# Kernel tuning notes

Measured on AMD Instinct MI355X. Metric: run time of the kernel, lower is better.

## Reference

```python
import jax, jax.numpy as jnp
import numpy as np

N_NODES = 100000
N_EDGES = 1600000
EMB_DIM = 32
NUM_LAYERS = 3


def setup_inputs() -> dict:
    key = jax.random.key(0)
    k_emb, k_w, k_row, k_col = jax.random.split(key, 4)
    emb = jax.random.normal(k_emb, (N_NODES, EMB_DIM), dtype=jnp.float32)
    # positive normalized edge weights (stands in for 1/sqrt(d1*d2))
    edge_weight = jax.random.uniform(k_w, (N_EDGES,), dtype=jnp.float32)
    row = jax.random.randint(k_row, (N_EDGES,), 0, N_NODES, dtype=jnp.int32)
    col = jax.random.randint(k_col, (N_EDGES,), 0, N_NODES, dtype=jnp.int32)
    return {"emb": emb, "edge_weight": edge_weight, "row": row, "col": col,
            "num_layers": NUM_LAYERS}


def reference(emb, edge_weight, row, col, num_layers):
    # Repeated SpMM: out[row] += w * X[col], equivalent to
    # torch.sparse.mm(sparse_coo(stack([row,col]), w, (N,N)), X)
    n = emb.shape[0]
    w = edge_weight[:, None]  # [E, 1]
    X = emb
    for _ in range(num_layers):
        msgs = w * X[col]  # gather + scale, [E, d]
        X = jax.ops.segment_sum(msgs, row, num_segments=n)
    return X
```

## Files before the change

kernel.cpp:

```cpp
#include <hip/hip_runtime.h>

#define EMB_DIM 32
#define CB_SHIFT 10
#define CB_ROWS 1024
#define COLBITS 17
#define OCT 8
#define EPB 4096
#define P1_T 256
#define SCAN_T 256
#define SCAN_E 8
#define SCAN_BLOCK (SCAN_T * SCAN_E)

__device__ __forceinline__ unsigned short f2b(float f) {
    unsigned u = __float_as_uint(f);
    u += 0x7fffu + ((u >> 16) & 1u);
    return (unsigned short)(u >> 16);
}
__device__ __forceinline__ unsigned f2b2(float lo, float hi) {
    return (unsigned)f2b(lo) | ((unsigned)f2b(hi) << 16);
}
__device__ __forceinline__ float blo(unsigned u) { return __uint_as_float(u << 16); }
__device__ __forceinline__ float bhi(unsigned u) { return __uint_as_float(u & 0xffff0000u); }


__global__ void coarse_count(const int* __restrict__ row, int* __restrict__ C,
                             int n_edges, int ncb, int nblk) {
    __shared__ int h[128];
    const int t = threadIdx.x;
    if (t < 128) h[t] = 0;
    __syncthreads();
    const int base = blockIdx.x * EPB;
    const int end = min(base + EPB, n_edges);
    for (int i = base + t; i < end; i += P1_T)
        atomicAdd(&h[row[i] >> CB_SHIFT], 1);
    __syncthreads();
    if (t < ncb) C[t * nblk + blockIdx.x] = h[t];
}


__global__ void scan_block_sums(const int* __restrict__ C, int* __restrict__ bsum, int M) {
    const int base = blockIdx.x * SCAN_BLOCK;
    const int t = threadIdx.x;
    int s = 0;
#pragma unroll
    for (int i = 0; i < SCAN_E; ++i) {
        int idx = base + i * SCAN_T + t;
        if (idx < M) s += C[idx];
    }
    __shared__ int red[SCAN_T];
    red[t] = s;
    __syncthreads();
    for (int d = SCAN_T / 2; d > 0; d >>= 1) {
        if (t < d) red[t] += red[t + d];
        __syncthreads();
    }
    if (t == 0) bsum[blockIdx.x] = red[0];
}

__global__ void scan_bsum(int* __restrict__ bsum, int nbs, int* __restrict__ off, int n_nodes) {
    __shared__ int sh[SCAN_T];
    const int t = threadIdx.x;
    int carry = 0;
    for (int base = 0; base < nbs; base += SCAN_T) {
        int v = (base + t < nbs) ? bsum[base + t] : 0;
        sh[t] = v;
        __syncthreads();
        for (int d = 1; d < SCAN_T; d <<= 1) {
            int add = (t >= d) ? sh[t - d] : 0;
            __syncthreads();
            sh[t] += add;
            __syncthreads();
        }
        if (base + t < nbs) bsum[base + t] = carry + sh[t] - v;
        int chunk_total = sh[SCAN_T - 1];
        __syncthreads();
        carry += chunk_total;
    }
    if (t == 0) off[n_nodes] = carry;
}

__global__ void scan_block_write(int* __restrict__ C, const int* __restrict__ bbase, int M) {
    const int base = blockIdx.x * SCAN_BLOCK;
    const int t = threadIdx.x;
    const int lo = base + t * SCAN_E;
    int vals[SCAN_E];
#pragma unroll
    for (int i = 0; i < SCAN_E; ++i) {
        int idx = lo + i;
        vals[i] = (idx < M) ? C[idx] : 0;
    }
    int tsum = 0;
#pragma unroll
    for (int i = 0; i < SCAN_E; ++i) tsum += vals[i];

    __shared__ int sh[SCAN_T];
    sh[t] = tsum;
    __syncthreads();
    for (int d = 1; d < SCAN_T; d <<= 1) {
        int add = (t >= d) ? sh[t - d] : 0;
        __syncthreads();
        sh[t] += add;
        __syncthreads();
    }
    int run = bbase[blockIdx.x] + sh[t] - tsum;
#pragma unroll
    for (int i = 0; i < SCAN_E; ++i) {
        int idx = lo + i;
        if (idx < M) C[idx] = run;
        run += vals[i];
    }
}

__global__ void coarse_scatter(const int* __restrict__ row, const int* __restrict__ col,
                               const float* __restrict__ w, const int* __restrict__ O,
                               int2* __restrict__ ebuf, int n_edges, int ncb, int nblk) {
    __shared__ int cur[128];
    const int t = threadIdx.x;
    if (t < ncb) cur[t] = O[t * nblk + blockIdx.x];
    __syncthreads();
    const int base = blockIdx.x * EPB;
    const int end = min(base + EPB, n_edges);
    for (int i = base + t; i < end; i += P1_T) {
        int r = row[i];
        int pos = atomicAdd(&cur[r >> CB_SHIFT], 1);
        ebuf[pos] = make_int2(((r & (CB_ROWS - 1)) << COLBITS) | col[i], __float_as_int(w[i]));
    }
}

__global__ void fine_localize(const int2* __restrict__ ebuf, const int* __restrict__ O,
                              int ncb, int nblk, int n_edges,
                              int2* __restrict__ colw, int* __restrict__ off, int n_nodes) {
    const int b = blockIdx.x;
    const int base = O[b * nblk];
    const int endp = (b + 1 < ncb) ? O[(b + 1) * nblk] : n_edges;
    const int t = threadIdx.x;

    __shared__ int cnt[CB_ROWS * OCT];
    __shared__ int cur[CB_ROWS * OCT];
    __shared__ int sh[CB_ROWS];

#pragma unroll
    for (int i = 0; i < OCT; ++i) cnt[t + i * CB_ROWS] = 0;
    __syncthreads();

    for (int i = base + t; i < endp; i += CB_ROWS) {
        int ex = ebuf[i].x;
        int bin = ((ex >> COLBITS) << 3) | ((ex >> 14) & 7);
        atomicAdd(&cnt[bin], 1);
    }
    __syncthreads();

    const int4* cnt4 = (const int4*)cnt;
    int4 a = cnt4[t * 2];
    int4 c = cnt4[t * 2 + 1];
    int loc[OCT] = {a.x, a.y, a.z, a.w, c.x, c.y, c.z, c.w};
    int s = 0;
#pragma unroll
    for (int i = 0; i < OCT; ++i) s += loc[i];
    sh[t] = s;
    __syncthreads();
    for (int d = 1; d < CB_ROWS; d <<= 1) {
        int add = (t >= d) ? sh[t - d] : 0;
        __syncthreads();
        sh[t] += add;
        __syncthreads();
    }
    int run = sh[t] - s;
    const int r = b * CB_ROWS + t;
    if (r < n_nodes) off[r] = base + run;
    int co[OCT];
#pragma unroll
    for (int i = 0; i < OCT; ++i) { co[i] = run; run += loc[i]; }
    int4* cur4 = (int4*)cur;
    cur4[t * 2]     = make_int4(co[0], co[1], co[2], co[3]);
    cur4[t * 2 + 1] = make_int4(co[4], co[5], co[6], co[7]);
    __syncthreads();

    for (int i = base + t; i < endp; i += CB_ROWS) {
        int2 ev = ebuf[i];
        int bin = ((ev.x >> COLBITS) << 3) | ((ev.x >> 14) & 7);
        int pos = base + atomicAdd(&cur[bin], 1);
        colw[pos] = make_int2(ev.x & ((1 << COLBITS) - 1), ev.y);
    }
}

__global__ void cvt_bf16(const float* __restrict__ in, unsigned short* __restrict__ out, int n4) {
    int i = blockIdx.x * blockDim.x + threadIdx.x;
    if (i >= n4) return;
    float4 v = reinterpret_cast<const float4*>(in)[i];
    ushort4 o;
    o.x = f2b(v.x); o.y = f2b(v.y); o.z = f2b(v.z); o.w = f2b(v.w);
    reinterpret_cast<ushort4*>(out)[i] = o;
}

template<bool OUT_BF16>
__global__ void spmv_bf(const unsigned* __restrict__ X, const int* __restrict__ off,
                        const int2* __restrict__ colw, void* __restrict__ outp,
                        int n_nodes) {
    long tid = (long)blockIdx.x * blockDim.x + threadIdx.x;
    int r = (int)(tid >> 2);
    int q = (int)(tid & 3);
    if (r >= n_nodes) return;

    const int start = off[r];
    const int end   = off[r + 1];

    float acc[8] = {0.f, 0.f, 0.f, 0.f, 0.f, 0.f, 0.f, 0.f};
    int k = start;
    for (; k + 4 <= end; k += 4) {
        int2 cw0 = colw[k + 0];
        int2 cw1 = colw[k + 1];
        int2 cw2 = colw[k + 2];
        int2 cw3 = colw[k + 3];
        uint4 h0 = *reinterpret_cast<const uint4*>(X + (size_t)cw0.x * 16 + q * 4);
        uint4 h1 = *reinterpret_cast<const uint4*>(X + (size_t)cw1.x * 16 + q * 4);
        uint4 h2 = *reinterpret_cast<const uint4*>(X + (size_t)cw2.x * 16 + q * 4);
        uint4 h3 = *reinterpret_cast<const uint4*>(X + (size_t)cw3.x * 16 + q * 4);
        const float w0 = __int_as_float(cw0.y), w1 = __int_as_float(cw1.y);
        const float w2 = __int_as_float(cw2.y), w3 = __int_as_float(cw3.y);
        acc[0] += w0 * blo(h0.x); acc[1] += w0 * bhi(h0.x);
        acc[2] += w0 * blo(h0.y); acc[3] += w0 * bhi(h0.y);
        acc[4] += w0 * blo(h0.z); acc[5] += w0 * bhi(h0.z);
        acc[6] += w0 * blo(h0.w); acc[7] += w0 * bhi(h0.w);
        acc[0] += w1 * blo(h1.x); acc[1] += w1 * bhi(h1.x);
        acc[2] += w1 * blo(h1.y); acc[3] += w1 * bhi(h1.y);
        acc[4] += w1 * blo(h1.z); acc[5] += w1 * bhi(h1.z);
        acc[6] += w1 * blo(h1.w); acc[7] += w1 * bhi(h1.w);
        acc[0] += w2 * blo(h2.x); acc[1] += w2 * bhi(h2.x);
        acc[2] += w2 * blo(h2.y); acc[3] += w2 * bhi(h2.y);
        acc[4] += w2 * blo(h2.z); acc[5] += w2 * bhi(h2.z);
        acc[6] += w2 * blo(h2.w); acc[7] += w2 * bhi(h2.w);
        acc[0] += w3 * blo(h3.x); acc[1] += w3 * bhi(h3.x);
        acc[2] += w3 * blo(h3.y); acc[3] += w3 * bhi(h3.y);
        acc[4] += w3 * blo(h3.z); acc[5] += w3 * bhi(h3.z);
        acc[6] += w3 * blo(h3.w); acc[7] += w3 * bhi(h3.w);
    }
    for (; k < end; ++k) {
        int2 cw = colw[k];
        const float wt = __int_as_float(cw.y);
        uint4 h = *reinterpret_cast<const uint4*>(X + (size_t)cw.x * 16 + q * 4);
        acc[0] += wt * blo(h.x); acc[1] += wt * bhi(h.x);
        acc[2] += wt * blo(h.y); acc[3] += wt * bhi(h.y);
        acc[4] += wt * blo(h.z); acc[5] += wt * bhi(h.z);
        acc[6] += wt * blo(h.w); acc[7] += wt * bhi(h.w);
    }
    if (OUT_BF16) {
        uint4 o;
        o.x = f2b2(acc[0], acc[1]);
        o.y = f2b2(acc[2], acc[3]);
        o.z = f2b2(acc[4], acc[5]);
        o.w = f2b2(acc[6], acc[7]);
        reinterpret_cast<uint4*>(outp)[(size_t)r * 4 + q] = o;
    } else {
        float4 lo4 = make_float4(acc[0], acc[1], acc[2], acc[3]);
        float4 hi4 = make_float4(acc[4], acc[5], acc[6], acc[7]);
        float4* o = reinterpret_cast<float4*>(outp) + (size_t)r * 8 + q * 2;
        o[0] = lo4;
        o[1] = hi4;
    }
}

__global__ void lightgcn_scatter(const float* __restrict__ X, const float* __restrict__ w,
                                 const int* __restrict__ row, const int* __restrict__ col,
                                 float* __restrict__ out, int n_edges) {
    long tid = (long)blockIdx.x * blockDim.x + threadIdx.x;
    int e = (int)(tid >> 3);
    int q = (int)(tid & 7);
    if (e >= n_edges) return;
    const int r = row[e];
    const int c = col[e];
    const float wt = w[e];
    const float4 v = *reinterpret_cast<const float4*>(X + (size_t)c * EMB_DIM + q * 4);
    float* o = out + (size_t)r * EMB_DIM + q * 4;
    atomicAdd(o + 0, wt * v.x);
    atomicAdd(o + 1, wt * v.y);
    atomicAdd(o + 2, wt * v.z);
    atomicAdd(o + 3, wt * v.w);
}

extern "C" void kernel_launch(void* const* d_in, const int* in_sizes, int n_in,
                              void* d_out, int out_size, void* d_ws, size_t ws_size,
                              hipStream_t stream) {
    const float* emb = (const float*)d_in[0];
    const float* w   = (const float*)d_in[1];
    const int*   row = (const int*)d_in[2];
    const int*   col = (const int*)d_in[3];

    const int n_nodes = in_sizes[0] / EMB_DIM;
    const int n_edges = in_sizes[1];

    float* out = (float*)d_out;
    const size_t xbytes = (size_t)n_nodes * EMB_DIM * sizeof(float);
    const size_t bfbytes = (size_t)n_nodes * EMB_DIM * 2;

    const int ncb  = (n_nodes + CB_ROWS - 1) / CB_ROWS;
    const int nblk = (n_edges + EPB - 1) / EPB;
    const int M    = ncb * nblk;
    const int nbs  = (M + SCAN_BLOCK - 1) / SCAN_BLOCK;

    const size_t ebuf_off = 0;
    size_t ebuf_sz = (size_t)n_edges * 8;
    if (ebuf_sz < 2 * bfbytes) ebuf_sz = 2 * bfbytes;
    ebuf_sz = (ebuf_sz + 15) & ~(size_t)15;
    const size_t colw_off = ebuf_off + ebuf_sz;
    const size_t colw_sz  = ((size_t)n_edges * 8 + 15) & ~(size_t)15;
    const size_t off_off  = colw_off + colw_sz;
    const size_t off_sz   = ((size_t)(n_nodes + 2) * 4 + 15) & ~(size_t)15;
    const size_t C_off    = off_off + off_sz;
    const size_t C_sz     = ((size_t)M * 4 + 15) & ~(size_t)15;
    const size_t bsum_off = C_off + C_sz;
    const size_t bsum_sz  = ((size_t)(nbs + 1) * 4 + 15) & ~(size_t)15;
    const size_t need     = bsum_off + bsum_sz;

    if (ws_size < need || ncb > 128) {
        float* tmp = (float*)d_ws;
        const int threads = 256;
        const int blocks = (int)(((long)n_edges * 8 + threads - 1) / threads);
        hipMemsetAsync(d_out, 0, xbytes, stream);
        lightgcn_scatter<<<blocks, threads, 0, stream>>>(emb, w, row, col, out, n_edges);
        hipMemsetAsync(d_ws, 0, xbytes, stream);
        lightgcn_scatter<<<blocks, threads, 0, stream>>>(out, w, row, col, tmp, n_edges);
        hipMemsetAsync(d_out, 0, xbytes, stream);
        lightgcn_scatter<<<blocks, threads, 0, stream>>>(tmp, w, row, col, out, n_edges);
        return;
    }

    char* ws = (char*)d_ws;
    int2*  ebuf = (int2*)(ws + ebuf_off);
    unsigned* Xb = (unsigned*)(ws + ebuf_off);
    unsigned* Yb = (unsigned*)(ws + ebuf_off + bfbytes);
    int2*  colw = (int2*)(ws + colw_off);
    int*   offs = (int*)(ws + off_off);
    int*   C    = (int*)(ws + C_off);
    int*   bsum = (int*)(ws + bsum_off);

    coarse_count<<<nblk, P1_T, 0, stream>>>(row, C, n_edges, ncb, nblk);
    scan_block_sums<<<nbs, SCAN_T, 0, stream>>>(C, bsum, M);
    scan_bsum<<<1, SCAN_T, 0, stream>>>(bsum, nbs, offs, n_nodes);
    scan_block_write<<<nbs, SCAN_T, 0, stream>>>(C, bsum, M);
    coarse_scatter<<<nblk, P1_T, 0, stream>>>(row, col, w, C, ebuf, n_edges, ncb, nblk);
    fine_localize<<<ncb, CB_ROWS, 0, stream>>>(ebuf, C, ncb, nblk, n_edges, colw, offs, n_nodes);

    const int threads = 256;
    const int n4 = n_nodes * EMB_DIM / 4;
    cvt_bf16<<<(n4 + threads - 1) / threads, threads, 0, stream>>>(emb, (unsigned short*)Xb, n4);

    const int rblocks = (int)(((long)n_nodes * 4 + threads - 1) / threads);
    spmv_bf<true ><<<rblocks, threads, 0, stream>>>(Xb, offs, colw, Yb,  n_nodes);
    spmv_bf<true ><<<rblocks, threads, 0, stream>>>(Yb, offs, colw, Xb,  n_nodes);
    spmv_bf<false><<<rblocks, threads, 0, stream>>>(Xb, offs, colw, out, n_nodes);
}
```

Baseline: 136.6 us.

## Shrink coarse row buckets to 128 rows for more fine_localize blocks

Coarse row buckets shrink from 1024 to 128 rows, so there are about 782 buckets instead of 98 and fine_localize launches many more blocks, each with 256 threads. The per-block histogram is now written block-major for coalesced writes, and the scan kernels read it transposed into a separate offsets array O. The aim is better GPU occupancy during the fine sort, which previously ran only about 98 large blocks. In exchange, coarse_scatter has far more shared-memory buckets with lower locality per bucket, and the scans process an M about eight times larger using strided, uncoalesced reads.

```diff
diff --git a/kernel.cpp b/kernel.cpp
--- a/kernel.cpp
+++ b/kernel.cpp
@@ -1,12 +1,13 @@
 #include <hip/hip_runtime.h>
 
 #define EMB_DIM 32
-#define CB_SHIFT 10
-#define CB_ROWS 1024
+#define CB_SHIFT 7
+#define CB_ROWS 128
 #define COLBITS 17
 #define OCT 8
 #define EPB 4096
 #define P1_T 256
+#define FL_T 256
 #define SCAN_T 256
 #define SCAN_E 8
 #define SCAN_BLOCK (SCAN_T * SCAN_E)
@@ -24,28 +25,34 @@
 
 
 __global__ void coarse_count(const int* __restrict__ row, int* __restrict__ C,
-                             int n_edges, int ncb, int nblk) {
-    __shared__ int h[128];
-    const int t = threadIdx.x;
-    if (t < 128) h[t] = 0;
+                             int n_edges, int ncb) {
+    __shared__ int h[1024];
+    const int t = threadIdx.x;
+    for (int idx = t; idx < ncb; idx += P1_T) h[idx] = 0;
     __syncthreads();
     const int base = blockIdx.x * EPB;
     const int end = min(base + EPB, n_edges);
     for (int i = base + t; i < end; i += P1_T)
         atomicAdd(&h[row[i] >> CB_SHIFT], 1);
     __syncthreads();
-    if (t < ncb) C[t * nblk + blockIdx.x] = h[t];
-}
-
-
-__global__ void scan_block_sums(const int* __restrict__ C, int* __restrict__ bsum, int M) {
+    for (int idx = t; idx < ncb; idx += P1_T)
+        C[(size_t)blockIdx.x * ncb + idx] = h[idx];
+}
+
+
+__global__ void scan_block_sums(const int* __restrict__ C, int* __restrict__ bsum,
+                                int M, int ncb, int nblk) {
     const int base = blockIdx.x * SCAN_BLOCK;
     const int t = threadIdx.x;
     int s = 0;
 #pragma unroll
     for (int i = 0; i < SCAN_E; ++i) {
-        int idx = base + i * SCAN_T + t;
-        if (idx < M) s += C[idx];
+        int p = base + i * SCAN_T + t;
+        if (p < M) {
+            int b = p / nblk;
+            int k = p - b * nblk;
+            s += C[(size_t)k * ncb + b];
+        }
     }
     __shared__ int red[SCAN_T];
     red[t] = s;
@@ -79,15 +86,21 @@
     if (t == 0) off[n_nodes] = carry;
 }
 
-__global__ void scan_block_write(int* __restrict__ C, const int* __restrict__ bbase, int M) {
-    const int base = blockIdx.x * SCAN_BLOCK;
-    const int t = threadIdx.x;
-    const int lo = base + t * SCAN_E;
+__global__ void scan_block_write(const int* __restrict__ C, const int* __restrict__ bbase,
+                                 int* __restrict__ O, int M, int ncb, int nblk) {
+    const int t = threadIdx.x;
+    const int lo = blockIdx.x * SCAN_BLOCK + t * SCAN_E;
     int vals[SCAN_E];
 #pragma unroll
     for (int i = 0; i < SCAN_E; ++i) {
-        int idx = lo + i;
-        vals[i] = (idx < M) ? C[idx] : 0;
+        int p = lo + i;
+        if (p < M) {
+            int b = p / nblk;
+            int k = p - b * nblk;
+            vals[i] = C[(size_t)k * ncb + b];
+        } else {
+            vals[i] = 0;
+        }
     }
     int tsum = 0;
 #pragma unroll
@@ -105,8 +118,8 @@
     int run = bbase[blockIdx.x] + sh[t] - tsum;
 #pragma unroll
     for (int i = 0; i < SCAN_E; ++i) {
-        int idx = lo + i;
-        if (idx < M) C[idx] = run;
+        int p = lo + i;
+        if (p < M) O[p] = run;
         run += vals[i];
     }
 }
@@ -114,9 +127,10 @@
 __global__ void coarse_scatter(const int* __restrict__ row, const int* __restrict__ col,
                                const float* __restrict__ w, const int* __restrict__ O,
                                int2* __restrict__ ebuf, int n_edges, int ncb, int nblk) {
-    __shared__ int cur[128];
-    const int t = threadIdx.x;
-    if (t < ncb) cur[t] = O[t * nblk + blockIdx.x];
+    __shared__ int cur[1024];
+    const int t = threadIdx.x;
+    for (int idx = t; idx < ncb; idx += P1_T)
+        cur[idx] = O[(size_t)idx * nblk + blockIdx.x];
     __syncthreads();
     const int base = blockIdx.x * EPB;
     const int end = min(base + EPB, n_edges);
@@ -131,52 +145,57 @@
                               int ncb, int nblk, int n_edges,
                               int2* __restrict__ colw, int* __restrict__ off, int n_nodes) {
     const int b = blockIdx.x;
-    const int base = O[b * nblk];
-    const int endp = (b + 1 < ncb) ? O[(b + 1) * nblk] : n_edges;
+    const int base = O[(size_t)b * nblk];
+    const int endp = (b + 1 < ncb) ? O[(size_t)(b + 1) * nblk] : n_edges;
     const int t = threadIdx.x;
 
     __shared__ int cnt[CB_ROWS * OCT];
     __shared__ int cur[CB_ROWS * OCT];
     __shared__ int sh[CB_ROWS];
 
-#pragma unroll
-    for (int i = 0; i < OCT; ++i) cnt[t + i * CB_ROWS] = 0;
-    __syncthreads();
-
-    for (int i = base + t; i < endp; i += CB_ROWS) {
+    for (int i = t; i < CB_ROWS * OCT; i += FL_T) cnt[i] = 0;
+    __syncthreads();
+
+    for (int i = base + t; i < endp; i += FL_T) {
         int ex = ebuf[i].x;
         int bin = ((ex >> COLBITS) << 3) | ((ex >> 14) & 7);
         atomicAdd(&cnt[bin], 1);
     }
     __syncthreads();
 
-    const int4* cnt4 = (const int4*)cnt;
-    int4 a = cnt4[t * 2];
-    int4 c = cnt4[t * 2 + 1];
-    int loc[OCT] = {a.x, a.y, a.z, a.w, c.x, c.y, c.z, c.w};
+    int loc[OCT];
     int s = 0;
-#pragma unroll
-    for (int i = 0; i < OCT; ++i) s += loc[i];
-    sh[t] = s;
+    if (t < CB_ROWS) {
+        const int4* cnt4 = (const int4*)cnt;
+        int4 a = cnt4[t * 2];
+        int4 c = cnt4[t * 2 + 1];
+        loc[0] = a.x; loc[1] = a.y; loc[2] = a.z; loc[3] = a.w;
+        loc[4] = c.x; loc[5] = c.y; loc[6] = c.z; loc[7] = c.w;
+#pragma unroll
+        for (int i = 0; i < OCT; ++i) s += loc[i];
+        sh[t] = s;
+    }
     __syncthreads();
     for (int d = 1; d < CB_ROWS; d <<= 1) {
-        int add = (t >= d) ? sh[t - d] : 0;
-        __syncthreads();
-        sh[t] += add;
-        __syncthreads();
-    }
-    int run = sh[t] - s;
-    const int r = b * CB_ROWS + t;
-    if (r < n_nodes) off[r] = base + run;
-    int co[OCT];
-#pragma unroll
-    for (int i = 0; i < OCT; ++i) { co[i] = run; run += loc[i]; }
-    int4* cur4 = (int4*)cur;
-    cur4[t * 2]     = make_int4(co[0], co[1], co[2], co[3]);
-    cur4[t * 2 + 1] = make_int4(co[4], co[5], co[6], co[7]);
-    __syncthreads();
-
-    for (int i = base + t; i < endp; i += CB_ROWS) {
+        int add = (t < CB_ROWS && t >= d) ? sh[t - d] : 0;
+        __syncthreads();
+        if (t < CB_ROWS) sh[t] += add;
+        __syncthreads();
+    }
+    if (t < CB_ROWS) {
+        int run = sh[t] - s;
+        const int r = b * CB_ROWS + t;
+        if (r < n_nodes) off[r] = base + run;
+        int co[OCT];
+#pragma unroll
+        for (int i = 0; i < OCT; ++i) { co[i] = run; run += loc[i]; }
+        int4* cur4 = (int4*)cur;
+        cur4[t * 2]     = make_int4(co[0], co[1], co[2], co[3]);
+        cur4[t * 2 + 1] = make_int4(co[4], co[5], co[6], co[7]);
+    }
+    __syncthreads();
+
+    for (int i = base + t; i < endp; i += FL_T) {
         int2 ev = ebuf[i];
         int bin = ((ev.x >> COLBITS) << 3) | ((ev.x >> 14) & 7);
         int pos = base + atomicAdd(&cur[bin], 1);
@@ -308,11 +327,13 @@
     const size_t off_sz   = ((size_t)(n_nodes + 2) * 4 + 15) & ~(size_t)15;
     const size_t C_off    = off_off + off_sz;
     const size_t C_sz     = ((size_t)M * 4 + 15) & ~(size_t)15;
-    const size_t bsum_off = C_off + C_sz;
+    const size_t O_off    = C_off + C_sz;
+    const size_t O_sz     = C_sz;
+    const size_t bsum_off = O_off + O_sz;
     const size_t bsum_sz  = ((size_t)(nbs + 1) * 4 + 15) & ~(size_t)15;
     const size_t need     = bsum_off + bsum_sz;
 
-    if (ws_size < need || ncb > 128) {
+    if (ws_size < need || ncb > 1024) {
         float* tmp = (float*)d_ws;
         const int threads = 256;
         const int blocks = (int)(((long)n_edges * 8 + threads - 1) / threads);
@@ -332,14 +353,15 @@
     int2*  colw = (int2*)(ws + colw_off);
     int*   offs = (int*)(ws + off_off);
     int*   C    = (int*)(ws + C_off);
+    int*   O    = (int*)(ws + O_off);
     int*   bsum = (int*)(ws + bsum_off);
 
-    coarse_count<<<nblk, P1_T, 0, stream>>>(row, C, n_edges, ncb, nblk);
-    scan_block_sums<<<nbs, SCAN_T, 0, stream>>>(C, bsum, M);
+    coarse_count<<<nblk, P1_T, 0, stream>>>(row, C, n_edges, ncb);
+    scan_block_sums<<<nbs, SCAN_T, 0, stream>>>(C, bsum, M, ncb, nblk);
     scan_bsum<<<1, SCAN_T, 0, stream>>>(bsum, nbs, offs, n_nodes);
-    scan_block_write<<<nbs, SCAN_T, 0, stream>>>(C, bsum, M);
-    coarse_scatter<<<nblk, P1_T, 0, stream>>>(row, col, w, C, ebuf, n_edges, ncb, nblk);
-    fine_localize<<<ncb, CB_ROWS, 0, stream>>>(ebuf, C, ncb, nblk, n_edges, colw, offs, n_nodes);
+    scan_block_write<<<nbs, SCAN_T, 0, stream>>>(C, bsum, O, M, ncb, nblk);
+    coarse_scatter<<<nblk, P1_T, 0, stream>>>(row, col, w, O, ebuf, n_edges, ncb, nblk);
+    fine_localize<<<ncb, FL_T, 0, stream>>>(ebuf, O, ncb, nblk, n_edges, colw, offs, n_nodes);
 
     const int threads = 256;
     const int n4 = n_nodes * EMB_DIM / 4;
```

Result: faster. 133.0 us (-2.6%).
